# Performance work log

Measured on AMD Instinct MI355X. Metric: run time of the kernel, lower is better.

The kernel has to match this reference:

```python
import jax, jax.numpy as jnp
import numpy as np

# dims
D = 1024; H = 16; DH = D // H; FF = 4096; E = 4; K = 64; M = 256; B = 2; S = 1024
DEPTH = 1.0 + 12.0 / 24.0 * 0.5  # depth_factor for layer_idx=12, num_layers=24
SCALE = 1.0 / np.sqrt(DH)
GATE_DIM = 128


def _heads(t):
    # (B,S,D) -> (B,H,S,DH)
    return t.reshape(t.shape[0], t.shape[1], H, DH).transpose(0, 2, 1, 3)


def _merge(t):
    # (B,H,S,DH) -> (B,S,D)
    return t.transpose(0, 2, 1, 3).reshape(t.shape[0], t.shape[2], D)


def _ln(x, g, b):
    mu = x.mean(-1, keepdims=True)
    var = x.var(-1, keepdims=True)
    return (x - mu) / jnp.sqrt(var + 1e-5) * g + b


def _mha(x, wq, bq, wk, bk, wv, bv, wo, bo):
    q = _heads(x @ wq + bq); k = _heads(x @ wk + bk); v = _heads(x @ wv + bv)
    s = jnp.einsum('bhqd,bhkd->bhqk', q, k) * SCALE
    a = jax.nn.softmax(s, axis=-1)
    return _merge(jnp.einsum('bhqk,bhkd->bhqd', a, v)) @ wo + bo


def _sparse_mha(x, wq, bq, wk, bk, wv, bv, wo, bo):
    # DynamicSparseAttention: keep top-K scores per query, mask the rest
    q = _heads(x @ wq + bq); k = _heads(x @ wk + bk); v = _heads(x @ wv + bv)
    s = jnp.einsum('bhqd,bhkd->bhqk', q, k) * SCALE
    thr = jax.lax.top_k(s, K)[0][..., -1:]             # kth-largest per query
    s = jnp.where(s >= thr, s, -1e9)
    a = jax.nn.softmax(s, axis=-1)
    return _merge(jnp.einsum('bhqk,bhkd->bhqd', a, v)) @ wo + bo


def _performer(x, wq, bq, wk, bk, wv, bv, wo, bo, wf):
    # LearnedPerformerAttention: learned ReLU feature maps, linear attention
    q = _heads(x @ wq + bq); k = _heads(x @ wk + bk); v = _heads(x @ wv + bv)
    pq = jax.nn.relu(jnp.einsum('bhsd,dm->bhsm', q, wf))
    pk = jax.nn.relu(jnp.einsum('bhsd,dm->bhsm', k, wf))
    kv = jnp.einsum('bhsm,bhsd->bhmd', pk, v)          # (B,H,M,DH)
    z = pk.sum(axis=2)                                  # (B,H,M)
    num = jnp.einsum('bhsm,bhmd->bhsd', pq, kv)
    den = jnp.einsum('bhsm,bhm->bhs', pq, z) + 1e-6
    return _merge(num / den[..., None]) @ wo + bo


def setup_inputs() -> dict:
    key = jax.random.key(0)
    ks = iter(jax.random.split(key, 64))

    def w(shape):
        fan_in = shape[-2] if len(shape) > 1 else shape[-1]
        return (jax.random.normal(next(ks), shape, jnp.float32) / np.sqrt(fan_in))

    inp = {'x': jax.random.normal(next(ks), (B, S, D), jnp.float32)}
    # AdaptiveReasoningGate
    inp['arg_w1'] = w((D, GATE_DIM)); inp['arg_b1'] = jnp.zeros(GATE_DIM)
    inp['arg_w2'] = w((GATE_DIM, 2)); inp['arg_b2'] = jnp.zeros(2)
    # MoE attention: router + per-expert MHA
    inp['moe_wr'] = w((D, E)); inp['moe_br'] = jnp.zeros(E)
    for n in ('wq', 'wk', 'wv', 'wo'):
        inp['moe_' + n] = w((E, D, D))
        inp['moe_b' + n[1]] = jnp.zeros((E, D))
    # sparse attention
    for n in ('wq', 'wk', 'wv', 'wo'):
        inp['sp_' + n] = w((D, D)); inp['sp_b' + n[1]] = jnp.zeros(D)
    # performer attention
    for n in ('wq', 'wk', 'wv', 'wo'):
        inp['pf_' + n] = w((D, D)); inp['pf_b' + n[1]] = jnp.zeros(D)
    inp['pf_wf'] = w((DH, M))
    # TAA gate, attention combiner gate
    inp['taa_wg'] = w((D, 2)); inp['taa_bg'] = jnp.zeros(2)
    inp['ag_w'] = w((D, 2)); inp['ag_b'] = jnp.zeros(2)
    # FFN
    inp['ffn_w1'] = w((D, FF)); inp['ffn_b1'] = jnp.zeros(FF)
    inp['ffn_w2'] = w((FF, D)); inp['ffn_b2'] = jnp.zeros(D)
    # norms
    for i in (1, 2, 3):
        inp[f'n{i}_g'] = jnp.ones(D); inp[f'n{i}_b'] = jnp.zeros(D)
    return inp


def _forward(x, arg_w1, arg_b1, arg_w2, arg_b2,
             moe_wr, moe_br, moe_wq, moe_bq, moe_wk, moe_bk, moe_wv, moe_bv, moe_wo, moe_bo,
             sp_wq, sp_bq, sp_wk, sp_bk, sp_wv, sp_bv, sp_wo, sp_bo,
             pf_wq, pf_bq, pf_wk, pf_bk, pf_wv, pf_bv, pf_wo, pf_bo, pf_wf,
             taa_wg, taa_bg, ag_w, ag_b,
             ffn_w1, ffn_b1, ffn_w2, ffn_b2,
             n1_g, n1_b, n2_g, n2_b, n3_g, n3_b):
    avg = x.mean(axis=1)  # (B,D)
    # AdaptiveReasoningGate (attn_weight computed but unused in original forward)
    gw = jax.nn.sigmoid(jax.nn.gelu(avg @ arg_w1 + arg_b1) @ arg_w2 + arg_b2)
    ffn_weight = gw[:, 1][:, None, None]
    # MoE attention: token-level softmax routing over E expert MHAs
    ex_out = jax.vmap(
        lambda wq, bq, wk, bk, wv, bv, wo, bo: _mha(x, wq, bq, wk, bk, wv, bv, wo, bo)
    )(moe_wq, moe_bq, moe_wk, moe_bk, moe_wv, moe_bv, moe_wo, moe_bo)  # (E,B,S,D)
    gates = jax.nn.softmax(x @ moe_wr + moe_br, axis=-1)               # (B,S,E)
    moe_out = jnp.einsum('ebsd,bse->bsd', ex_out, gates)
    # Hybrid thought-aware attention (dropout = identity, eval mode)
    sp = _sparse_mha(x, sp_wq, sp_bq, sp_wk, sp_bk, sp_wv, sp_bv, sp_wo, sp_bo)
    pf = _performer(x, pf_wq, pf_bq, pf_wk, pf_bk, pf_wv, pf_bv, pf_wo, pf_bo, pf_wf)
    tg = jax.nn.softmax(avg @ taa_wg + taa_bg, axis=-1)
    taa_out = tg[:, 0][:, None, None] * sp + tg[:, 1][:, None, None] * pf
    # gated combine of MoE and TAA paths
    ag = jax.nn.softmax(avg @ ag_w + ag_b, axis=-1)
    attn_out = (ag[:, 0][:, None, None] * moe_out + ag[:, 1][:, None, None] * taa_out) * DEPTH
    x1 = _ln(x + attn_out, n1_g, n1_b)
    ffn_out = (jax.nn.gelu(x1 @ ffn_w1 + ffn_b1) @ ffn_w2 + ffn_b2) * ffn_weight * DEPTH
    x2 = _ln(x1 + ffn_out, n2_g, n2_b)
    return _ln(x2, n3_g, n3_b)


def reference(x, arg_w1, arg_b1, arg_w2, arg_b2,
              moe_wr, moe_br, moe_wq, moe_bq, moe_wk, moe_bk, moe_wv, moe_bv, moe_wo, moe_bo,
              sp_wq, sp_bq, sp_wk, sp_bk, sp_wv, sp_bv, sp_wo, sp_bo,
              pf_wq, pf_bq, pf_wk, pf_bk, pf_wv, pf_bv, pf_wo, pf_bo, pf_wf,
              taa_wg, taa_bg, ag_w, ag_b,
              ffn_w1, ffn_b1, ffn_w2, ffn_b2,
              n1_g, n1_b, n2_g, n2_b, n3_g, n3_b):
    return _forward(x, arg_w1, arg_b1, arg_w2, arg_b2,
                    moe_wr, moe_br, moe_wq, moe_bq, moe_wk, moe_bk, moe_wv, moe_bv, moe_wo, moe_bo,
                    sp_wq, sp_bq, sp_wk, sp_bk, sp_wv, sp_bv, sp_wo, sp_bo,
                    pf_wq, pf_bq, pf_wk, pf_bk, pf_wv, pf_bv, pf_wo, pf_bo, pf_wf,
                    taa_wg, taa_bg, ag_w, ag_b,
                    ffn_w1, ffn_b1, ffn_w2, ffn_b2,
                    n1_g, n1_b, n2_g, n2_b, n3_g, n3_b)
```

## Files before the change

### kernel.cpp

```cpp
#include <hip/hip_runtime.h>
#include <hip/hip_bf16.h>
#include <math.h>

#define Bq 2
#define Sq 1024
#define Dq 1024
#define Hq 16
#define DHq 64
#define FFq 4096
#define Eq 4
#define Kq 64
#define Mq 256
#define GATEq 128
#define BSq (Bq*Sq)
#define DEPTHF 1.25f
#define SCALEF 0.125f
#define DD (Dq*Dq)
#define PLANE ((size_t)BSq*Dq)

typedef __hip_bfloat16 bf16;
typedef __attribute__((ext_vector_type(8))) __bf16 bf16x8;
typedef __attribute__((ext_vector_type(4))) float f32x4;

__device__ __forceinline__ float toF(float v){ return v; }
__device__ __forceinline__ float toF(bf16 v){ return __bfloat162float(v); }
__device__ __forceinline__ void stF(float* p, size_t i, float v){ p[i] = v; }
__device__ __forceinline__ void stF(bf16* p, size_t i, float v){ p[i] = __float2bfloat16(v); }
__device__ __forceinline__ float gelu_f(float x){
  const float c = 0.7978845608028654f;
  return 0.5f*x*(1.0f + tanhf(c*(x + 0.044715f*x*x*x)));
}
__device__ __forceinline__ unsigned short bfb(float f){
  bf16 h = __float2bfloat16(f);
  return *(unsigned short*)&h;
}
__device__ __forceinline__ float thr_decode(unsigned c){
  unsigned ub = (c & 0x80000000u) ? (c & 0x7FFFFFFFu) : ~c;
  return __uint_as_float(ub);
}
__device__ __forceinline__ void async_lds16(const void* g, void* lds) {
  __builtin_amdgcn_global_load_lds(
      (const __attribute__((address_space(1))) void*)(unsigned long long)(uintptr_t)g,
      (__attribute__((address_space(3))) void*)(unsigned)(uintptr_t)lds, 16, 0, 0);
}

__global__ __launch_bounds__(256)
void detect_kernel(const unsigned* __restrict__ xw, int* __restrict__ flag)
{
  __shared__ int cnt;
  if (threadIdx.x == 0) cnt = 0;
  __syncthreads();
  int c = 0;
  for (int i = threadIdx.x; i < 4096; i += 256) {
    unsigned e = (xw[i] >> 7) & 0xFFu;
    c += (e >= 0x70u && e <= 0x8Fu) ? 1 : 0;
  }
#pragma unroll
  for (int o = 32; o >= 1; o >>= 1) c += __shfl_xor(c, o);
  if ((threadIdx.x & 63) == 0) atomicAdd(&cnt, c);
  __syncthreads();
  if (threadIdx.x == 0) *flag = (cnt > 2048) ? 1 : 0;
}

__global__ __launch_bounds__(256)
void conv_x_kernel(const int* __restrict__ flag, const void* __restrict__ x, bf16* __restrict__ xb)
{
  int f = *flag;
  int i0 = (blockIdx.x*256 + threadIdx.x)*4;
  if (i0 >= BSq*Dq) return;
  if (f) {
    const bf16* s = (const bf16*)x;
#pragma unroll
    for (int k=0;k<4;k++) xb[i0+k] = s[i0+k];
  } else {
    const float* s = (const float*)x;
#pragma unroll
    for (int k=0;k<4;k++) xb[i0+k] = __float2bfloat16(s[i0+k]);
  }
}

template<typename IT>
__device__ void packseg(bf16* dst, const IT* src, int len)
{
  for (int i = threadIdx.x; i < len; i += 256) dst[i] = __float2bfloat16(toF(src[i]));
}
__global__ __launch_bounds__(256)
void pack_bias_kernel(const int* __restrict__ flag, bf16* arena,
    const void* bq, const void* bk, const void* bv, const void* bo,
    const void* sq, const void* sk, const void* sv, const void* so,
    const void* pq, const void* pk, const void* pv, const void* po,
    const void* f1, const void* f2)
{
  int f = *flag;
  if (f) {
    packseg(arena+0,     (const bf16*)bq, 4096); packseg(arena+4096,  (const bf16*)bk, 4096);
    packseg(arena+8192,  (const bf16*)bv, 4096); packseg(arena+12288, (const bf16*)bo, 4096);
    packseg(arena+16384, (const bf16*)sq, 1024); packseg(arena+17408, (const bf16*)sk, 1024);
    packseg(arena+18432, (const bf16*)sv, 1024); packseg(arena+19456, (const bf16*)so, 1024);
    packseg(arena+20480, (const bf16*)pq, 1024); packseg(arena+21504, (const bf16*)pk, 1024);
    packseg(arena+22528, (const bf16*)pv, 1024); packseg(arena+23552, (const bf16*)po, 1024);
// ... 5 lines not shown
    packseg(arena+18432, (const float*)sv, 1024); packseg(arena+19456, (const float*)so, 1024);
    packseg(arena+20480, (const float*)pq, 1024); packseg(arena+21504, (const float*)pk, 1024);
    packseg(arena+22528, (const float*)pv, 1024); packseg(arena+23552, (const float*)po, 1024);
    packseg(arena+24576, (const float*)f1, 4096); packseg(arena+28672, (const float*)f2, 1024);
  }
}

template<typename IT>
__device__ void packwft_body(const IT* __restrict__ wf, bf16* __restrict__ wft)
{
  int i = blockIdx.x*256 + threadIdx.x;
  if (i >= DHq*Mq) return;
  int d = i >> 8, m = i & 255;
  wft[m*DHq + d] = __float2bfloat16(toF(wf[(size_t)d*Mq + m]));
}
__global__ __launch_bounds__(256)
void pack_wft_kernel(const int* __restrict__ flag, const void* wf, bf16* wft)
{
  if (*flag) packwft_body<bf16>((const bf16*)wf, wft);
  else       packwft_body<float>((const float*)wf, wft);
}

template<typename WT>
__device__ void gemm_core(bf16* As, unsigned* Bs,
    const bf16* __restrict__ A, int lda, const WT* __restrict__ W,
    const bf16* __restrict__ barena, int biasOff,
    const float* __restrict__ rowscale, bf16* __restrict__ C,
    float* __restrict__ Cf, int N, int K, int act)
{
  int tid = threadIdx.x;
  int lane = tid & 63, wave = tid >> 6;
  int wr = wave >> 1, wc = wave & 1;
  int bm = blockIdx.x * 128, bn = blockIdx.y * 128;

  int arow1 = wave*16 + (lane>>2);
  int akey = (arow1 >> 1) & 3;
  int acol = ((lane & 3) ^ akey) * 8;
  const bf16* aP1 = A + (size_t)(bm + arow1)*lda + acol;
  const bf16* aP2 = A + (size_t)(bm + arow1 + 64)*lda + acol;

  int kp = tid >> 4, nb8 = (tid & 15)*8;
  const WT* wP = W + (size_t)(2*kp)*N + bn + nb8;

  f32x4 acc[4][4];
#pragma unroll
  for (int i=0;i<4;i++)
#pragma unroll
    for (int j=0;j<4;j++) acc[i][j] = (f32x4){0.f,0.f,0.f,0.f};

  int m = lane & 15, q = lane >> 4;
  int akey2 = (m >> 1) & 3;
  int aq = (q ^ akey2) * 8;

  const int T = K >> 5;
  uint4 rwa, rwb, rwc, rwd;

// ... 76 lines not shown
#pragma unroll
  for (int i=0;i<4;i++) {
    int row0 = bm + wr*64 + i*16 + q*4;
#pragma unroll
    for (int j=0;j<4;j++) {
      int col = bn + wc*64 + j*16 + m;
      float bvv = barena ? toF(barena[biasOff + col]) : 0.f;
#pragma unroll
      for (int r=0;r<4;r++) {
        size_t idx = (size_t)(row0 + r)*N + col;
        if (Cf) {
          Cf[idx] = acc[i][j][r];
        } else {
          float v = acc[i][j][r] + bvv;
          if (act) v = gelu_f(v);
          if (rowscale) v *= rowscale[row0 + r];
          C[idx] = __float2bfloat16(v);
        }
      }
    }
  }
}

__global__ __launch_bounds__(256, 3)
void gemm6_k(const int* __restrict__ flag, const bf16* Abase, long az,
    const void* w0, const void* w1, const void* w2,
    const void* w3, const void* w4, const void* w5,
    long e0, long e1, long e2, long e3, long e4, long e5,
    int b0, int b1, int b2, int b3, int b4, int b5,
    const float* r0, const float* r1, const float* r2,
    const float* r3, const float* r4, const float* r5,
    bf16* c0, bf16* c1, bf16* c2, bf16* c3, bf16* c4, bf16* c5,
    const bf16* barena, int N, int K)
{
  __shared__ bf16 As[2*4096];
  __shared__ unsigned Bs[2*2112];
  int z = blockIdx.z;
  const void* Wp = (z==0)?w0:(z==1)?w1:(z==2)?w2:(z==3)?w3:(z==4)?w4:w5;
  long eo        = (z==0)?e0:(z==1)?e1:(z==2)?e2:(z==3)?e3:(z==4)?e4:e5;
  int bo         = (z==0)?b0:(z==1)?b1:(z==2)?b2:(z==3)?b3:(z==4)?b4:b5;
  const float* rs= (z==0)?r0:(z==1)?r1:(z==2)?r2:(z==3)?r3:(z==4)?r4:r5;
  bf16* C        = (z==0)?c0:(z==1)?c1:(z==2)?c2:(z==3)?c3:(z==4)?c4:c5;
  const bf16* A  = Abase + (size_t)z*az;
  if (*flag) gemm_core<bf16>(As, Bs, A, K, (const bf16*)Wp + eo, barena, bo, rs, C, nullptr, N, K, 0);
  else       gemm_core<float>(As, Bs, A, K, (const float*)Wp + eo, barena, bo, rs, C, nullptr, N, K, 0);
}

__global__ __launch_bounds__(256, 3)
void gemm1_k(const int* __restrict__ flag, const bf16* A, int lda, const void* W,
             const bf16* barena, int biasOff, const float* rowscale,
             bf16* C, float* Cf, long cfz, int N, int K, int act, int kz)
{
  __shared__ bf16 As[2*4096];
  __shared__ unsigned Bs[2*2112];
  int z = blockIdx.z;
  const bf16* Az = A + (size_t)z*kz;
  long wo = (size_t)z*kz*N;
  float* Cfz = Cf ? (Cf + (size_t)z*cfz) : nullptr;
  if (*flag) gemm_core<bf16>(As, Bs, Az, lda, (const bf16*)W + wo, barena, biasOff, rowscale, C, Cfz, N, K, act);
  else       gemm_core<float>(As, Bs, Az, lda, (const float*)W + wo, barena, biasOff, rowscale, C, Cfz, N, K, act);
}

__global__ __launch_bounds__(256)
void combine_ffn2(const float* __restrict__ pf, const bf16* __restrict__ barena,
                  const float* __restrict__ rs, bf16* __restrict__ out)
{
  int i0 = (blockIdx.x*256 + threadIdx.x)*4;
  float4 s0 = *(const float4*)(pf + i0);
  float4 s1 = *(const float4*)(pf + PLANE + i0);
  float4 s2 = *(const float4*)(pf + 2*PLANE + i0);
  float4 s3 = *(const float4*)(pf + 3*PLANE + i0);
  int row = i0 >> 10, col = i0 & 1023;
  float r = rs[row];
  out[i0+0] = __float2bfloat16((s0.x+s1.x+s2.x+s3.x + toF(barena[28672+col+0])) * r);
  out[i0+1] = __float2bfloat16((s0.y+s1.y+s2.y+s3.y + toF(barena[28672+col+1])) * r);
  out[i0+2] = __float2bfloat16((s0.z+s1.z+s2.z+s3.z + toF(barena[28672+col+2])) * r);
  out[i0+3] = __float2bfloat16((s0.w+s1.w+s2.w+s3.w + toF(barena[28672+col+3])) * r);
}

__global__ __launch_bounds__(256)
void vtrans_kernel(const bf16* __restrict__ Vb, long vz, bf16* __restrict__ Vtb, long vtz)
{
  __shared__ bf16 t[64][72];
  const bf16* V = Vb + (size_t)blockIdx.z*vz;
  bf16* Vt = Vtb + (size_t)blockIdx.z*vtz;
  int bh = blockIdx.x;
  int sc_ = blockIdx.y;
  int b = bh >> 4, h = bh & 15;
  int tid = threadIdx.x;
  {
    int s = tid >> 2, dd = (tid & 3) * 16;
    const bf16* src = &V[((size_t)b*Sq + sc_*64 + s)*Dq + h*64 + dd];
    uint4 a0 = *(const uint4*)src;
    uint4 a1 = *(const uint4*)(src + 8);
    *(uint4*)&t[s][dd]     = a0;
    *(uint4*)&t[s][dd + 8] = a1;
  }
  __syncthreads();
  {
    int d = tid >> 2, sp = (tid & 3) * 16;
// ... 118 lines not shown
  lrun += __shfl_xor(lrun, 32);
#pragma unroll
  for (int dt=0;dt<4;dt++)
    *(float4*)&ocs[wave][m][dt*16 + q*4] = (float4){oc[dt][0], oc[dt][1], oc[dt][2], oc[dt][3]};
  if (q == 0) { mls[wave][0][m] = mrun; mls[wave][1][m] = lrun; }
  __syncthreads();

  int mm = tid >> 4, d0 = (tid & 15) * 4;
  float m0 = mls[0][0][mm], m1 = mls[1][0][mm], m2 = mls[2][0][mm], m3 = mls[3][0][mm];
  float M = fmaxf(fmaxf(m0, m1), fmaxf(m2, m3));
  float a0 = __expf(m0 - M), a1 = __expf(m1 - M), a2 = __expf(m2 - M), a3 = __expf(m3 - M);
  float l = mls[0][1][mm]*a0 + mls[1][1][mm]*a1 + mls[2][1][mm]*a2 + mls[3][1][mm]*a3;
  l = fmaxf(l, 1e-30f);
  float inv = 1.0f / l;
  float4 o0 = *(const float4*)&ocs[0][mm][d0];
  float4 o1 = *(const float4*)&ocs[1][mm][d0];
  float4 o2 = *(const float4*)&ocs[2][mm][d0];
  float4 o3 = *(const float4*)&ocs[3][mm][d0];
  float r0 = (o0.x*a0 + o1.x*a1 + o2.x*a2 + o3.x*a3) * inv;
  float r1 = (o0.y*a0 + o1.y*a1 + o2.y*a2 + o3.y*a3) * inv;
  float r2 = (o0.z*a0 + o1.z*a1 + o2.z*a2 + o3.z*a3) * inv;
  float r3 = (o0.w*a0 + o1.w*a1 + o2.w*a2 + o3.w*a3) * inv;
  bf16* op = O + base + (size_t)(q0 + mm)*Dq + d0;
  unsigned w0 = (unsigned)bfb(r0) | ((unsigned)bfb(r1) << 16);
  unsigned w1 = (unsigned)bfb(r2) | ((unsigned)bfb(r3) << 16);
  *(uint2*)op = make_uint2(w0, w1);
}

template<int SPARSE>
__global__ __launch_bounds__(256, 4)
void attn_kernel(const bf16* __restrict__ Q, const bf16* __restrict__ K,
                 const bf16* __restrict__ Vt, bf16* __restrict__ O)
{
  const int PAST = 1032;
  __shared__ bf16 pa[16*PAST];
  __shared__ float partA[64], partB[64];
  __shared__ int cntb[2][64];

  int p_ = blockIdx.x;
  int g_ = (p_ & 7)*4 + ((p_ >> 3) & 3);
  int rb = p_ >> 5;
  int h  = g_ & 15;
  int b  = g_ >> 4;
  int tid = threadIdx.x, lane = tid & 63, wave = tid >> 6;
  int m = lane & 15, q = lane >> 4;
  size_t base = ((size_t)b*Sq)*Dq + (size_t)h*DHq;
  int q0 = rb*16;

  const bf16* qrow = &Q[base + (size_t)(q0+m)*Dq + q*8];
  bf16x8 aq0 = *(const bf16x8*)qrow;
  bf16x8 aq1 = *(const bf16x8*)(qrow + 32);

  f32x4 cc[16];
#pragma unroll
  for (int t = 0; t < 16; t++) {
    int j0 = wave*256 + t*16;
    const bf16* kp = &K[base + (size_t)(j0+m)*Dq + q*8];
    bf16x8 b0 = *(const bf16x8*)kp;
    bf16x8 b1 = *(const bf16x8*)(kp + 32);
    f32x4 c = {0.f,0.f,0.f,0.f};
    c = __builtin_amdgcn_mfma_f32_16x16x32_bf16(aq0, b0, c, 0, 0, 0);
    c = __builtin_amdgcn_mfma_f32_16x16x32_bf16(aq1, b1, c, 0, 0, 0);
#pragma unroll
    for (int r=0;r<4;r++) c[r] *= SCALEF;
    cc[t] = c;
  }

  unsigned lo[4] = {0u,0u,0u,0u};
  if (SPARSE) {
    int cnt_cur[4] = {Sq, Sq, Sq, Sq};
    for (int bit = 31; bit >= 0; bit--) {
      int par = bit & 1;
      unsigned cand[4];
      float candf[4];
      int c4[4] = {0,0,0,0};
#pragma unroll
      for (int r=0;r<4;r++) {
        cand[r] = lo[r] | (1u << bit);
        candf[r] = thr_decode(cand[r]);
      }
#pragma unroll
      for (int t=0;t<16;t++)
#pragma unroll
        for (int r=0;r<4;r++) c4[r] += (cc[t][r] >= candf[r]) ? 1 : 0;
#pragma unroll
      for (int o=1;o<16;o<<=1)
#pragma unroll
        for (int r=0;r<4;r++) c4[r] += __shfl_xor(c4[r], o);
      if (m == 0) {
#pragma unroll
        for (int r=0;r<4;r++) cntb[par][wave*16 + q*4 + r] = c4[r];
      }
      __syncthreads();
      int done = 1;
#pragma unroll
      for (int r=0;r<4;r++) {
        int row = q*4 + r;
        int tot = cntb[par][row] + cntb[par][16+row] + cntb[par][32+row] + cntb[par][48+row];
        if (tot >= Kq) { lo[r] = cand[r]; cnt_cur[r] = tot; }
        done &= (cnt_cur[r] == Kq) ? 1 : 0;
      }
      done &= __shfl_xor(done, 16);
      done &= __shfl_xor(done, 32);
      if (done) break;
    }
  }

  float mrow[4];
#pragma unroll
  for (int r=0;r<4;r++) {
    float v = -1e30f;
#pragma unroll
    for (int t=0;t<16;t++) v = fmaxf(v, cc[t][r]);
#pragma unroll
    for (int o=1;o<16;o<<=1) v = fmaxf(v, __shfl_xor(v, o));
    mrow[r] = v;
  }
  if (m == 0) {
#pragma unroll
    for (int r=0;r<4;r++) partA[wave*16 + q*4 + r] = mrow[r];
  }
  __syncthreads();
// ... 207 lines not shown

  const bf16* kvp = kvb + (size_t)bh*(DHq*Mq);
  f32x4 oc[4];
#pragma unroll
  for (int dt=0;dt<4;dt++) oc[dt] = (f32x4){0.f,0.f,0.f,0.f};
#pragma unroll
  for (int ks=0; ks<8; ks++) {
    bf16x8 ap = *(const bf16x8*)&pa2[(wave*16 + ml)*PQST + ks*32 + q*8];
#pragma unroll
    for (int dt=0;dt<4;dt++) {
      bf16x8 bk = *(const bf16x8*)&kvp[(size_t)(dt*16 + ml)*Mq + ks*32 + q*8];
      oc[dt] = __builtin_amdgcn_mfma_f32_16x16x32_bf16(ap, bk, oc[dt], 0, 0, 0);
    }
  }
#pragma unroll
  for (int dt=0;dt<4;dt++)
#pragma unroll
    for (int r=0;r<4;r++)
      O[base + (size_t)(s0 + wave*16 + q*4 + r)*Dq + dt*16 + ml] =
          __float2bfloat16(oc[dt][r] / den[r]);
}

template<typename IT>
__device__ void ln_body(float* buf, float* red, const IT* __restrict__ xb,
                        const void* Ap, const void* Bp,
                        const IT* __restrict__ g, const IT* __restrict__ be,
                        void* out, int mode)
{
  int row = blockIdx.x;
  int tid = threadIdx.x;
  size_t off = (size_t)row*Dq;
  for (int dd = tid; dd < Dq; dd += 256) {
    float v;
    if (mode == 0)      v = toF(xb[off+dd]) + toF(((const bf16*)Ap)[off+dd]);
    else if (mode == 1) v = toF(((const bf16*)Ap)[off+dd]) + toF(((const bf16*)Bp)[off+dd]);
    else if (mode == 3) {
      const bf16* P = (const bf16*)Ap;
      v = toF(xb[off+dd]);
#pragma unroll
      for (int p=0;p<6;p++) v += toF(P[(size_t)p*PLANE + off + dd]);
    }
    else                v = toF(((const bf16*)Ap)[off+dd]);
    buf[dd] = v;
  }
  __syncthreads();
  float s = 0.f, q = 0.f;
  for (int dd = tid; dd < Dq; dd += 256) { float v = buf[dd]; s += v; q += v*v; }
#pragma unroll
  for (int o=32;o>=1;o>>=1) { s += __shfl_xor(s,o); q += __shfl_xor(q,o); }
  int w = tid >> 6;
  if ((tid & 63) == 0) { red[w] = s; red[4+w] = q; }
  __syncthreads();
  if (tid == 0) {
    float S1 = red[0]+red[1]+red[2]+red[3];
    float Q1 = red[4]+red[5]+red[6]+red[7];
    float mu = S1 / (float)Dq;
    float var = Q1 / (float)Dq - mu*mu;
    red[8] = mu; red[9] = rsqrtf(fmaxf(var, 0.f) + 1e-5f);
  }
  __syncthreads();
  float mu = red[8], inv = red[9];
  for (int dd = tid; dd < Dq; dd += 256) {
    float v = (buf[dd]-mu)*inv*toF(g[dd]) + toF(be[dd]);
    if (mode == 2) stF((IT*)out, off+dd, v);
    else           stF((bf16*)out, off+dd, v);
  }
}

__global__ __launch_bounds__(256)
void ln_kernel(const int* __restrict__ flag, const void* xb, const void* A, const void* Bv,
               const void* g, const void* be, void* out, int mode)
{
  __shared__ float buf[Dq];
  __shared__ float red[10];
  if (*flag) ln_body<bf16>(buf, red, (const bf16*)xb, A, Bv, (const bf16*)g, (const bf16*)be, out, mode);
  else       ln_body<float>(buf, red, (const float*)xb, A, Bv, (const float*)g, (const float*)be, out, mode);
}

__global__ __launch_bounds__(256)
void avg2_kernel(const int* __restrict__ flag, const void* __restrict__ x, float* __restrict__ avgsum)
{
  int b  = blockIdx.x >> 4;
  int sc = blockIdx.x & 15;
  int t = threadIdx.x;
  int c0 = t*4;
  float a0=0.f,a1=0.f,a2=0.f,a3=0.f;
  if (*flag) {
    const unsigned* X = (const unsigned*)x;
    for (int s = sc*64; s < sc*64+64; s++) {
      size_t bi = (((size_t)(b*Sq + s))*Dq + c0) >> 1;
      unsigned u0 = X[bi], u1 = X[bi+1];
      a0 += __uint_as_float(u0 << 16);
      a1 += __uint_as_float(u0 & 0xFFFF0000u);
      a2 += __uint_as_float(u1 << 16);
      a3 += __uint_as_float(u1 & 0xFFFF0000u);
    }
  } else {
    const float* X = (const float*)x;
    for (int s = sc*64; s < sc*64+64; s++) {
// ... 83 lines not shown
    float ag0 = f0*inv, ag1 = f1*inv;
    cmb0[b] = ag0*DEPTHF;
    sh[2+b] = tg0*ag1*DEPTHF;
    sh[4+b] = tg1*ag1*DEPTHF;
    sh[6+b] = sh[b]*DEPTHF;
  }
  __syncthreads();
  for (int i = tid; i < BSq; i += 256) {
    int b = i >> 10;
    rs_tg0[i] = sh[2+b]; rs_tg1[i] = sh[4+b]; rs_ffn[i] = sh[6+b];
  }
}
__global__ __launch_bounds__(256)
void gate_fin_kernel(const int* __restrict__ flag, const float* g1b, const float* lgb,
    const void* w2, const void* b2, float* cmb0,
    float* rs_tg0, float* rs_tg1, float* rs_ffn)
{
  __shared__ float sh[8];
  if (*flag) gfin_body<bf16>(sh, g1b, lgb, (const bf16*)w2, (const bf16*)b2, cmb0, rs_tg0, rs_tg1, rs_ffn);
  else       gfin_body<float>(sh, g1b, lgb, (const float*)w2, (const float*)b2, cmb0, rs_tg0, rs_tg1, rs_ffn);
}

template<typename IT>
__device__ void router_body(const IT* __restrict__ x, const IT* __restrict__ wr,
                            const IT* __restrict__ br, const float* __restrict__ cmb0,
                            float* __restrict__ gates_t)
{
  int row = blockIdx.x;
  int tid = threadIdx.x;
  size_t off = (size_t)row*Dq;
  float a0=0,a1=0,a2=0,a3=0;
  for (int dd = tid; dd < Dq; dd += 64) {
    float xv = toF(x[off+dd]);
    a0 += xv*toF(wr[dd*Eq+0]);
    a1 += xv*toF(wr[dd*Eq+1]);
    a2 += xv*toF(wr[dd*Eq+2]);
    a3 += xv*toF(wr[dd*Eq+3]);
  }
#pragma unroll
  for (int o=32;o>=1;o>>=1) {
    a0 += __shfl_xor(a0,o); a1 += __shfl_xor(a1,o);
    a2 += __shfl_xor(a2,o); a3 += __shfl_xor(a3,o);
  }
  if (tid == 0) {
    a0 += toF(br[0]); a1 += toF(br[1]); a2 += toF(br[2]); a3 += toF(br[3]);
    float m = fmaxf(fmaxf(a0,a1),fmaxf(a2,a3));
    float e0=__expf(a0-m), e1=__expf(a1-m), e2=__expf(a2-m), e3=__expf(a3-m);
    float inv = 1.f/(e0+e1+e2+e3);
    float sc = cmb0[row >> 10];
    gates_t[0*BSq+row]=e0*inv*sc; gates_t[1*BSq+row]=e1*inv*sc;
    gates_t[2*BSq+row]=e2*inv*sc; gates_t[3*BSq+row]=e3*inv*sc;
  }
}
__global__ __launch_bounds__(64)
void router_kernel(const int* __restrict__ flag, const void* x, const void* wr,
                   const void* br, const float* cmb0, float* gates_t)
{
  if (*flag) router_body<bf16>((const bf16*)x, (const bf16*)wr, (const bf16*)br, cmb0, gates_t);
  else       router_body<float>((const float*)x, (const float*)wr, (const float*)br, cmb0, gates_t);
}

extern "C" void kernel_launch(void* const* d_in, const int* in_sizes, int n_in,
                              void* d_out, int out_size, void* d_ws, size_t ws_size,
                              hipStream_t stream) {
  const void* x      = d_in[0];
  const void* arg_w1 = d_in[1];  const void* arg_b1 = d_in[2];
  const void* arg_w2 = d_in[3];  const void* arg_b2 = d_in[4];
  const void* moe_wr = d_in[5];  const void* moe_br = d_in[6];
  const void* moe_wq = d_in[7];  const void* moe_bq = d_in[8];
  const void* moe_wk = d_in[9];  const void* moe_bk = d_in[10];
  const void* moe_wv = d_in[11]; const void* moe_bv = d_in[12];
  const void* moe_wo = d_in[13]; const void* moe_bo = d_in[14];
  const void* sp_wq  = d_in[15]; const void* sp_bq  = d_in[16];
  const void* sp_wk  = d_in[17]; const void* sp_bk  = d_in[18];
  const void* sp_wv  = d_in[19]; const void* sp_bv  = d_in[20];
  const void* sp_wo  = d_in[21]; const void* sp_bo  = d_in[22];
  const void* pf_wq  = d_in[23]; const void* pf_bq  = d_in[24];
  const void* pf_wk  = d_in[25]; const void* pf_bk  = d_in[26];
  const void* pf_wv  = d_in[27]; const void* pf_bv  = d_in[28];
  const void* pf_wo  = d_in[29]; const void* pf_bo  = d_in[30];
  const void* pf_wf  = d_in[31];
  const void* taa_wg = d_in[32]; const void* taa_bg = d_in[33];
  const void* ag_w   = d_in[34]; const void* ag_b   = d_in[35];
  const void* ffn_w1 = d_in[36]; const void* ffn_b1 = d_in[37];
  const void* ffn_w2 = d_in[38]; const void* ffn_b2 = d_in[39];
  const void* n1_g   = d_in[40]; const void* n1_b   = d_in[41];
  const void* n2_g   = d_in[42]; const void* n2_b   = d_in[43];
  const void* n3_g   = d_in[44]; const void* n3_b   = d_in[45];

  char* w = (char*)d_ws;
  const size_t MB = 1024*1024;
  bf16* xb  = (bf16*)w;
  bf16* Qp  = (bf16*)(w + 4*MB);
  bf16* KV  = (bf16*)(w + 28*MB);
  bf16* Vt  = (bf16*)(w + 44*MB);
  bf16* Pp  = (bf16*)(w + 28*MB);
  bf16* x1    = (bf16*)(w + 4*MB);
  bf16* ffn_h = (bf16*)(w + 8*MB);
  float* partF= (float*)(w + 24*MB);
  bf16* tmpb  = (bf16*)w;
  bf16* x2    = (bf16*)w;
  char* book = w + 56*MB;
  float* rs_tg0 = (float*)book;
  float* rs_tg1 = rs_tg0 + BSq;
  float* rs_ffn = rs_tg1 + BSq;
  float* cmb0   = rs_ffn + BSq;
  float* avgp   = cmb0 + 16;
  float* gates_t= avgp + Bq*Dq;
  float* zb     = gates_t + Eq*BSq;
  float* g1b    = zb + Bq*Hq*Mq;
  float* lgb    = g1b + 256;
  int*   dflag  = (int*)(lgb + 8);
  bf16*  barena = (bf16*)(dflag + 16);
  bf16*  wft    = barena + 29696;
  bf16*  kvb    = (bf16*)(w + 57*MB);

  detect_kernel<<<1, 256, 0, stream>>>((const unsigned*)x, dflag);
  hipMemsetAsync(avgp, 0, (size_t)(Bq*Dq)*sizeof(float), stream);
  conv_x_kernel<<<BSq*Dq/1024, 256, 0, stream>>>(dflag, x, xb);
  pack_bias_kernel<<<1, 256, 0, stream>>>(dflag, barena,
      moe_bq, moe_bk, moe_bv, moe_bo, sp_bq, sp_bk, sp_bv, sp_bo,
      pf_bq, pf_bk, pf_bv, pf_bo, ffn_b1, ffn_b2);
  pack_wft_kernel<<<64, 256, 0, stream>>>(dflag, pf_wf, wft);
  avg2_kernel<<<Bq*16, 256, 0, stream>>>(dflag, x, avgp);
  gate_dots_kernel<<<66, 256, 0, stream>>>(dflag, avgp, arg_w1, arg_b1,
      taa_wg, taa_bg, ag_w, ag_b, g1b, lgb);
  gate_fin_kernel<<<1, 256, 0, stream>>>(dflag, g1b, lgb, arg_w2, arg_b2,
      cmb0, rs_tg0, rs_tg1, rs_ffn);
  router_kernel<<<BSq, 64, 0, stream>>>(dflag, x, moe_wr, moe_br, cmb0, gates_t);

  dim3 g6(16, 8, 6);
  dim3 gVT(Bq*Hq, Sq/64, 2);
  int nAttnBlk = Bq*Hq*(Sq/16);
  int nFlashBlk = Bq*Hq*(Sq/16);

  for (int p = 0; p < 2; p++) {
    int e0 = 2*p, e1 = 2*p + 1;
    gemm6_k<<<g6, 256, 0, stream>>>(dflag, xb, 0L,
        moe_wq, moe_wk, moe_wv, moe_wq, moe_wk, moe_wv,
        (long)e0*DD, (long)e0*DD, (long)e0*DD, (long)e1*DD, (long)e1*DD, (long)e1*DD,
        e0*1024, e0*1024+4096, e0*1024+8192, e1*1024, e1*1024+4096, e1*1024+8192,
        nullptr, nullptr, nullptr, nullptr, nullptr, nullptr,
        Qp + (size_t)e0*PLANE, KV, KV + PLANE,
        Qp + (size_t)e1*PLANE, KV + 2*PLANE, KV + 3*PLANE,
        barena, Dq, Dq);
    vtrans_kernel<<<gVT, 256, 0, stream>>>(KV + PLANE, (long)(2*PLANE), Vt, (long)PLANE);
    flash_attn_kernel<<<nFlashBlk, 256, 0, stream>>>(Qp + (size_t)e0*PLANE, KV, Vt, Qp + (size_t)e0*PLANE);
    flash_attn_kernel<<<nFlashBlk, 256, 0, stream>>>(Qp + (size_t)e1*PLANE, KV + 2*PLANE, Vt + PLANE, Qp + (size_t)e1*PLANE);
  }

  gemm6_k<<<g6, 256, 0, stream>>>(dflag, xb, 0L,
      sp_wq, sp_wk, sp_wv, pf_wq, pf_wk, pf_wv,
      0L, 0L, 0L, 0L, 0L, 0L,
      16384, 17408, 18432, 20480, 21504, 22528,
      nullptr, nullptr, nullptr, nullptr, nullptr, nullptr,
      Qp + 4*PLANE, KV, KV + PLANE,
      Qp + 5*PLANE, KV + 2*PLANE, KV + 3*PLANE,
      barena, Dq, Dq);
  vtrans_kernel<<<gVT, 256, 0, stream>>>(KV + PLANE, (long)(2*PLANE), Vt, (long)PLANE);
  attn_kernel<1><<<nAttnBlk, 256, 0, stream>>>(Qp + 4*PLANE, KV, Vt, Qp + 4*PLANE);
  {
    dim3 gKV1(Bq*Hq, 8);
    perf_kv_mfma<<<gKV1, 256, 0, stream>>>(KV + 2*PLANE, Vt + PLANE, wft, kvb, zb);
  }
  perf_out_mfma<<<Bq*Hq*16, 256, 0, stream>>>(Qp + 5*PLANE, wft, kvb, zb, Qp + 5*PLANE);

  gemm6_k<<<g6, 256, 0, stream>>>(dflag, Qp, (long)PLANE,
      moe_wo, moe_wo, moe_wo, moe_wo, sp_wo, pf_wo,
      0L, (long)DD, (long)2*DD, (long)3*DD, 0L, 0L,
      12288, 13312, 14336, 15360, 19456, 23552,
      gates_t, gates_t + BSq, gates_t + 2*BSq, gates_t + 3*BSq, rs_tg0, rs_tg1,
      Pp, Pp + PLANE, Pp + 2*PLANE, Pp + 3*PLANE, Pp + 4*PLANE, Pp + 5*PLANE,
      barena, Dq, Dq);

  ln_kernel<<<BSq, 256, 0, stream>>>(dflag, x, Pp, nullptr, n1_g, n1_b, x1, 3);

  gemm1_k<<<dim3(16, 32, 1), 256, 0, stream>>>(dflag, x1, Dq, ffn_w1,
      barena, 24576, nullptr, ffn_h, nullptr, 0L, FFq, Dq, 1, 0);
  gemm1_k<<<dim3(16, 8, 4), 256, 0, stream>>>(dflag, ffn_h, FFq, ffn_w2,
      nullptr, 0, nullptr, nullptr, partF, (long)PLANE, Dq, 1024, 0, 1024);
  combine_ffn2<<<BSq*Dq/1024, 256, 0, stream>>>(partF, barena, rs_ffn, tmpb);

  ln_kernel<<<BSq, 256, 0, stream>>>(dflag, nullptr, x1, tmpb, n2_g, n2_b, x2, 1);
  ln_kernel<<<BSq, 256, 0, stream>>>(dflag, nullptr, x2, nullptr, n3_g, n3_b, d_out, 2);
}
```

Baseline: 1.092 ms.

## Fuse FFN tail layernorms, swizzle GEMM tiles across XCDs, radix-4 top-k search

Several independent changes land together. The FFN2 partial-sum combine and the two final layernorms merge into one kernel, which removes intermediate bf16 round trips and two launches. GEMM blocks are remapped so each XCD works on contiguous panels for better L2 reuse. The sparse attention threshold search now tests two bits per pass with three candidates, halving the sync rounds. LN1, the router and the x conversion are also vectorized with 4-wide loads and stores. Dropping the bf16 intermediate between FFN add and LN2 slightly changes numerics.

```diff
diff --git a/kernel.cpp b/kernel.cpp
--- a/kernel.cpp
+++ b/kernel.cpp
@@ -24,8 +24,6 @@
 
 __device__ __forceinline__ float toF(float v){ return v; }
 __device__ __forceinline__ float toF(bf16 v){ return __bfloat162float(v); }
-__device__ __forceinline__ void stF(float* p, size_t i, float v){ p[i] = v; }
-__device__ __forceinline__ void stF(bf16* p, size_t i, float v){ p[i] = __float2bfloat16(v); }
 __device__ __forceinline__ float gelu_f(float x){
   const float c = 0.7978845608028654f;
   return 0.5f*x*(1.0f + tanhf(c*(x + 0.044715f*x*x*x)));
@@ -33,6 +31,25 @@
 __device__ __forceinline__ unsigned short bfb(float f){
   bf16 h = __float2bfloat16(f);
   return *(unsigned short*)&h;
+}
+__device__ __forceinline__ uint2 pack4bf(float a, float b, float c, float d){
+  return make_uint2((unsigned)bfb(a) | ((unsigned)bfb(b) << 16),
+                    (unsigned)bfb(c) | ((unsigned)bfb(d) << 16));
+}
+template<typename IT>
+__device__ __forceinline__ void ld4(const IT* p, float* o){
+  if constexpr (sizeof(IT)==4){
+    float4 v = *(const float4*)p; o[0]=v.x; o[1]=v.y; o[2]=v.z; o[3]=v.w;
+  } else {
+    uint2 u = *(const uint2*)p;
+    o[0]=__uint_as_float(u.x<<16); o[1]=__uint_as_float(u.x&0xFFFF0000u);
+    o[2]=__uint_as_float(u.y<<16); o[3]=__uint_as_float(u.y&0xFFFF0000u);
+  }
+}
+template<typename IT>
+__device__ __forceinline__ void st4(IT* p, const float* v){
+  if constexpr (sizeof(IT)==4){ *(float4*)p = (float4){v[0],v[1],v[2],v[3]}; }
+  else { *(uint2*)p = pack4bf(v[0],v[1],v[2],v[3]); }
 }
 __device__ __forceinline__ float thr_decode(unsigned c){
   unsigned ub = (c & 0x80000000u) ? (c & 0x7FFFFFFFu) : ~c;
@@ -65,17 +82,13 @@
 __global__ __launch_bounds__(256)
 void conv_x_kernel(const int* __restrict__ flag, const void* __restrict__ x, bf16* __restrict__ xb)
 {
-  int f = *flag;
   int i0 = (blockIdx.x*256 + threadIdx.x)*4;
   if (i0 >= BSq*Dq) return;
-  if (f) {
-    const bf16* s = (const bf16*)x;
-#pragma unroll
-    for (int k=0;k<4;k++) xb[i0+k] = s[i0+k];
+  if (*flag) {
+    *(uint2*)(xb + i0) = *(const uint2*)((const bf16*)x + i0);
   } else {
-    const float* s = (const float*)x;
-#pragma unroll
-    for (int k=0;k<4;k++) xb[i0+k] = __float2bfloat16(s[i0+k]);
+    float4 v = *(const float4*)((const float*)x + i0);
+    *(uint2*)(xb + i0) = pack4bf(v.x, v.y, v.z, v.w);
   }
 }
 
@@ -127,7 +140,7 @@
 }
 
 template<typename WT>
-__device__ void gemm_core(bf16* As, unsigned* Bs,
+__device__ void gemm_core(bf16* As, unsigned* Bs, int bm, int bn,
     const bf16* __restrict__ A, int lda, const WT* __restrict__ W,
     const bf16* __restrict__ barena, int biasOff,
     const float* __restrict__ rowscale, bf16* __restrict__ C,
@@ -136,7 +149,6 @@
   int tid = threadIdx.x;
   int lane = tid & 63, wave = tid >> 6;
   int wr = wave >> 1, wc = wave & 1;
-  int bm = blockIdx.x * 128, bn = blockIdx.y * 128;
 
   int arow1 = wave*16 + (lane>>2);
   int akey = (arow1 >> 1) & 3;
@@ -259,6 +271,19 @@
   }
 }
 
+__device__ __forceinline__ void xcd_swizzle(int& xt, int& y, int& z)
+{
+  int nx = gridDim.x, ny = gridDim.y, nz = gridDim.z;
+  int lin = blockIdx.x + nx*(blockIdx.y + ny*blockIdx.z);
+  int ppx = (ny*nz) >> 3;
+  int xcd = lin & 7, sdx = lin >> 3;
+  int pp = sdx / nx;
+  xt = sdx - pp*nx;
+  int panel = xcd*ppx + pp;
+  y = panel % ny;
+  z = panel / ny;
+}
+
 __global__ __launch_bounds__(256, 3)
 void gemm6_k(const int* __restrict__ flag, const bf16* Abase, long az,
     const void* w0, const void* w1, const void* w2,
@@ -272,15 +297,16 @@
 {
   __shared__ bf16 As[2*4096];
   __shared__ unsigned Bs[2*2112];
-  int z = blockIdx.z;
+  int xt, y, z;
+  xcd_swizzle(xt, y, z);
   const void* Wp = (z==0)?w0:(z==1)?w1:(z==2)?w2:(z==3)?w3:(z==4)?w4:w5;
   long eo        = (z==0)?e0:(z==1)?e1:(z==2)?e2:(z==3)?e3:(z==4)?e4:e5;
   int bo         = (z==0)?b0:(z==1)?b1:(z==2)?b2:(z==3)?b3:(z==4)?b4:b5;
   const float* rs= (z==0)?r0:(z==1)?r1:(z==2)?r2:(z==3)?r3:(z==4)?r4:r5;
   bf16* C        = (z==0)?c0:(z==1)?c1:(z==2)?c2:(z==3)?c3:(z==4)?c4:c5;
   const bf16* A  = Abase + (size_t)z*az;
-  if (*flag) gemm_core<bf16>(As, Bs, A, K, (const bf16*)Wp + eo, barena, bo, rs, C, nullptr, N, K, 0);
-  else       gemm_core<float>(As, Bs, A, K, (const float*)Wp + eo, barena, bo, rs, C, nullptr, N, K, 0);
+  if (*flag) gemm_core<bf16>(As, Bs, xt*128, y*128, A, K, (const bf16*)Wp + eo, barena, bo, rs, C, nullptr, N, K, 0);
+  else       gemm_core<float>(As, Bs, xt*128, y*128, A, K, (const float*)Wp + eo, barena, bo, rs, C, nullptr, N, K, 0);
 }
 
 __global__ __launch_bounds__(256, 3)
@@ -290,29 +316,13 @@
 {
   __shared__ bf16 As[2*4096];
   __shared__ unsigned Bs[2*2112];
-  int z = blockIdx.z;
+  int xt, y, z;
+  xcd_swizzle(xt, y, z);
   const bf16* Az = A + (size_t)z*kz;
   long wo = (size_t)z*kz*N;
   float* Cfz = Cf ? (Cf + (size_t)z*cfz) : nullptr;
-  if (*flag) gemm_core<bf16>(As, Bs, Az, lda, (const bf16*)W + wo, barena, biasOff, rowscale, C, Cfz, N, K, act);
-  else       gemm_core<float>(As, Bs, Az, lda, (const float*)W + wo, barena, biasOff, rowscale, C, Cfz, N, K, act);
-}
-
-__global__ __launch_bounds__(256)
-void combine_ffn2(const float* __restrict__ pf, const bf16* __restrict__ barena,
-                  const float* __restrict__ rs, bf16* __restrict__ out)
-{
-  int i0 = (blockIdx.x*256 + threadIdx.x)*4;
-  float4 s0 = *(const float4*)(pf + i0);
-  float4 s1 = *(const float4*)(pf + PLANE + i0);
-  float4 s2 = *(const float4*)(pf + 2*PLANE + i0);
-  float4 s3 = *(const float4*)(pf + 3*PLANE + i0);
-  int row = i0 >> 10, col = i0 & 1023;
-  float r = rs[row];
-  out[i0+0] = __float2bfloat16((s0.x+s1.x+s2.x+s3.x + toF(barena[28672+col+0])) * r);
-  out[i0+1] = __float2bfloat16((s0.y+s1.y+s2.y+s3.y + toF(barena[28672+col+1])) * r);
-  out[i0+2] = __float2bfloat16((s0.z+s1.z+s2.z+s3.z + toF(barena[28672+col+2])) * r);
-  out[i0+3] = __float2bfloat16((s0.w+s1.w+s2.w+s3.w + toF(barena[28672+col+3])) * r);
+  if (*flag) gemm_core<bf16>(As, Bs, xt*128, y*128, Az, lda, (const bf16*)W + wo, barena, biasOff, rowscale, C, Cfz, N, K, act);
+  else       gemm_core<float>(As, Bs, xt*128, y*128, Az, lda, (const float*)W + wo, barena, biasOff, rowscale, C, Cfz, N, K, act);
 }
 
 __global__ __launch_bounds__(256)
@@ -477,9 +487,7 @@
   float r2 = (o0.z*a0 + o1.z*a1 + o2.z*a2 + o3.z*a3) * inv;
   float r3 = (o0.w*a0 + o1.w*a1 + o2.w*a2 + o3.w*a3) * inv;
   bf16* op = O + base + (size_t)(q0 + mm)*Dq + d0;
-  unsigned w0 = (unsigned)bfb(r0) | ((unsigned)bfb(r1) << 16);
-  unsigned w1 = (unsigned)bfb(r2) | ((unsigned)bfb(r3) << 16);
-  *(uint2*)op = make_uint2(w0, w1);
+  *(uint2*)op = pack4bf(r0, r1, r2, r3);
 }
 
 template<int SPARSE>
@@ -490,7 +498,7 @@
   const int PAST = 1032;
   __shared__ bf16 pa[16*PAST];
   __shared__ float partA[64], partB[64];
-  __shared__ int cntb[2][64];
+  __shared__ int cntb[2][192];
 
   int p_ = blockIdx.x;
   int g_ = (p_ & 7)*4 + ((p_ >> 3) & 3);
@@ -524,35 +532,50 @@
   unsigned lo[4] = {0u,0u,0u,0u};
   if (SPARSE) {
     int cnt_cur[4] = {Sq, Sq, Sq, Sq};
-    for (int bit = 31; bit >= 0; bit--) {
-      int par = bit & 1;
-      unsigned cand[4];
-      float candf[4];
-      int c4[4] = {0,0,0,0};
+    for (int bit = 30; bit >= 0; bit -= 2) {
+      int par = (bit >> 1) & 1;
+      float cf[4][3];
+      unsigned cd[4][3];
+      int cnt[4][3];
 #pragma unroll
       for (int r=0;r<4;r++) {
-        cand[r] = lo[r] | (1u << bit);
-        candf[r] = thr_decode(cand[r]);
+        cd[r][0] = lo[r] | (3u << bit);
+        cd[r][1] = lo[r] | (2u << bit);
+        cd[r][2] = lo[r] | (1u << bit);
+#pragma unroll
+        for (int c=0;c<3;c++) { cf[r][c] = thr_decode(cd[r][c]); cnt[r][c] = 0; }
       }
 #pragma unroll
       for (int t=0;t<16;t++)
 #pragma unroll
-        for (int r=0;r<4;r++) c4[r] += (cc[t][r] >= candf[r]) ? 1 : 0;
+        for (int r=0;r<4;r++) {
+          float v = cc[t][r];
+#pragma unroll
+          for (int c=0;c<3;c++) cnt[r][c] += (v >= cf[r][c]) ? 1 : 0;
+        }
 #pragma unroll
       for (int o=1;o<16;o<<=1)
 #pragma unroll
-        for (int r=0;r<4;r++) c4[r] += __shfl_xor(c4[r], o);
+        for (int r=0;r<4;r++)
+#pragma unroll
+          for (int c=0;c<3;c++) cnt[r][c] += __shfl_xor(cnt[r][c], o);
       if (m == 0) {
 #pragma unroll
-        for (int r=0;r<4;r++) cntb[par][wave*16 + q*4 + r] = c4[r];
+        for (int r=0;r<4;r++)
+#pragma unroll
+          for (int c=0;c<3;c++) cntb[par][c*64 + wave*16 + q*4 + r] = cnt[r][c];
       }
       __syncthreads();
       int done = 1;
 #pragma unroll
       for (int r=0;r<4;r++) {
         int row = q*4 + r;
-        int tot = cntb[par][row] + cntb[par][16+row] + cntb[par][32+row] + cntb[par][48+row];
-        if (tot >= Kq) { lo[r] = cand[r]; cnt_cur[r] = tot; }
+        int n3 = cntb[par][row] + cntb[par][16+row] + cntb[par][32+row] + cntb[par][48+row];
+        int n2 = cntb[par][64+row] + cntb[par][80+row] + cntb[par][96+row] + cntb[par][112+row];
+        int n1 = cntb[par][128+row] + cntb[par][144+row] + cntb[par][160+row] + cntb[par][176+row];
+        if      (n3 >= Kq) { lo[r] = cd[r][0]; cnt_cur[r] = n3; }
+        else if (n2 >= Kq) { lo[r] = cd[r][1]; cnt_cur[r] = n2; }
+        else if (n1 >= Kq) { lo[r] = cd[r][2]; cnt_cur[r] = n1; }
         done &= (cnt_cur[r] == Kq) ? 1 : 0;
       }
       done &= __shfl_xor(done, 16);
@@ -806,36 +829,29 @@
 }
 
 template<typename IT>
-__device__ void ln_body(float* buf, float* red, const IT* __restrict__ xb,
-                        const void* Ap, const void* Bp,
-                        const IT* __restrict__ g, const IT* __restrict__ be,
-                        void* out, int mode)
-{
-  int row = blockIdx.x;
-  int tid = threadIdx.x;
-  size_t off = (size_t)row*Dq;
-  for (int dd = tid; dd < Dq; dd += 256) {
-    float v;
-    if (mode == 0)      v = toF(xb[off+dd]) + toF(((const bf16*)Ap)[off+dd]);
-    else if (mode == 1) v = toF(((const bf16*)Ap)[off+dd]) + toF(((const bf16*)Bp)[off+dd]);
-    else if (mode == 3) {
-      const bf16* P = (const bf16*)Ap;
-      v = toF(xb[off+dd]);
-#pragma unroll
-      for (int p=0;p<6;p++) v += toF(P[(size_t)p*PLANE + off + dd]);
-    }
-    else                v = toF(((const bf16*)Ap)[off+dd]);
-    buf[dd] = v;
-  }
-  __syncthreads();
-  float s = 0.f, q = 0.f;
-  for (int dd = tid; dd < Dq; dd += 256) { float v = buf[dd]; s += v; q += v*v; }
-#pragma unroll
-  for (int o=32;o>=1;o>>=1) { s += __shfl_xor(s,o); q += __shfl_xor(q,o); }
-  int w = tid >> 6;
-  if ((tid & 63) == 0) { red[w] = s; red[4+w] = q; }
-  __syncthreads();
-  if (tid == 0) {
+__device__ void ln1_body(float* red, const IT* __restrict__ xsrc, const bf16* __restrict__ Pp,
+                         const IT* __restrict__ g, const IT* __restrict__ be, bf16* __restrict__ out)
+{
+  int row = blockIdx.x, t = threadIdx.x;
+  int c0 = t*4;
+  size_t off = (size_t)row*Dq + c0;
+  float v[4];
+  ld4(xsrc + off, v);
+#pragma unroll
+  for (int p=0;p<6;p++) {
+    float pv[4];
+    ld4(Pp + (size_t)p*PLANE + off, pv);
+#pragma unroll
+    for (int j=0;j<4;j++) v[j] += pv[j];
+  }
+  float s = v[0]+v[1]+v[2]+v[3];
+  float qq = v[0]*v[0]+v[1]*v[1]+v[2]*v[2]+v[3]*v[3];
+#pragma unroll
+  for (int o=32;o>=1;o>>=1) { s += __shfl_xor(s,o); qq += __shfl_xor(qq,o); }
+  int w = t >> 6;
+  if ((t & 63) == 0) { red[w] = s; red[4+w] = qq; }
+  __syncthreads();
+  if (t == 0) {
     float S1 = red[0]+red[1]+red[2]+red[3];
     float Q1 = red[4]+red[5]+red[6]+red[7];
     float mu = S1 / (float)Dq;
@@ -844,21 +860,97 @@
   }
   __syncthreads();
   float mu = red[8], inv = red[9];
-  for (int dd = tid; dd < Dq; dd += 256) {
-    float v = (buf[dd]-mu)*inv*toF(g[dd]) + toF(be[dd]);
-    if (mode == 2) stF((IT*)out, off+dd, v);
-    else           stF((bf16*)out, off+dd, v);
-  }
-}
-
-__global__ __launch_bounds__(256)
-void ln_kernel(const int* __restrict__ flag, const void* xb, const void* A, const void* Bv,
-               const void* g, const void* be, void* out, int mode)
-{
-  __shared__ float buf[Dq];
+  float gv[4], bv[4];
+  ld4(g + c0, gv); ld4(be + c0, bv);
+  float o_[4];
+#pragma unroll
+  for (int j=0;j<4;j++) o_[j] = (v[j]-mu)*inv*gv[j] + bv[j];
+  *(uint2*)(out + off) = pack4bf(o_[0], o_[1], o_[2], o_[3]);
+}
+__global__ __launch_bounds__(256)
+void ln1_kernel(const int* __restrict__ flag, const void* xsrc, const bf16* Pp,
+                const void* g, const void* be, bf16* out)
+{
   __shared__ float red[10];
-  if (*flag) ln_body<bf16>(buf, red, (const bf16*)xb, A, Bv, (const bf16*)g, (const bf16*)be, out, mode);
-  else       ln_body<float>(buf, red, (const float*)xb, A, Bv, (const float*)g, (const float*)be, out, mode);
+  if (*flag) ln1_body<bf16>(red, (const bf16*)xsrc, Pp, (const bf16*)g, (const bf16*)be, out);
+  else       ln1_body<float>(red, (const float*)xsrc, Pp, (const float*)g, (const float*)be, out);
+}
+
+template<typename IT>
+__device__ void ffntail_body(float* red, const float* __restrict__ pf,
+    const bf16* __restrict__ barena, const float* __restrict__ rs,
+    const bf16* __restrict__ x1,
+    const IT* __restrict__ g2, const IT* __restrict__ b2,
+    const IT* __restrict__ g3, const IT* __restrict__ b3, IT* __restrict__ out)
+{
+  int row = blockIdx.x, t = threadIdx.x;
+  int c0 = t*4;
+  size_t off = (size_t)row*Dq + c0;
+  float4 s0 = *(const float4*)(pf + off);
+  float4 s1 = *(const float4*)(pf + PLANE + off);
+  float4 s2 = *(const float4*)(pf + 2*PLANE + off);
+  float4 s3 = *(const float4*)(pf + 3*PLANE + off);
+  float bb[4]; ld4(barena + 28672 + c0, bb);
+  float xv[4]; ld4(x1 + off, xv);
+  float r = rs[row];
+  float v[4];
+  v[0] = xv[0] + (s0.x+s1.x+s2.x+s3.x + bb[0])*r;
+  v[1] = xv[1] + (s0.y+s1.y+s2.y+s3.y + bb[1])*r;
+  v[2] = xv[2] + (s0.z+s1.z+s2.z+s3.z + bb[2])*r;
+  v[3] = xv[3] + (s0.w+s1.w+s2.w+s3.w + bb[3])*r;
+  float s = v[0]+v[1]+v[2]+v[3];
+  float qq = v[0]*v[0]+v[1]*v[1]+v[2]*v[2]+v[3]*v[3];
+#pragma unroll
+  for (int o=32;o>=1;o>>=1) { s += __shfl_xor(s,o); qq += __shfl_xor(qq,o); }
+  int w = t >> 6;
+  if ((t & 63) == 0) { red[w] = s; red[4+w] = qq; }
+  __syncthreads();
+  if (t == 0) {
+    float S1 = red[0]+red[1]+red[2]+red[3];
+    float Q1 = red[4]+red[5]+red[6]+red[7];
+    float mu = S1 / (float)Dq;
+    float var = Q1 / (float)Dq - mu*mu;
+    red[8] = mu; red[9] = rsqrtf(fmaxf(var, 0.f) + 1e-5f);
+  }
+  __syncthreads();
+  float mu = red[8], inv = red[9];
+  float g2v[4], b2v[4];
+  ld4(g2 + c0, g2v); ld4(b2 + c0, b2v);
+  float y[4];
+#pragma unroll
+  for (int j=0;j<4;j++) y[j] = (v[j]-mu)*inv*g2v[j] + b2v[j];
+  float s2_ = y[0]+y[1]+y[2]+y[3];
+  float q2_ = y[0]*y[0]+y[1]*y[1]+y[2]*y[2]+y[3]*y[3];
+#pragma unroll
+  for (int o=32;o>=1;o>>=1) { s2_ += __shfl_xor(s2_,o); q2_ += __shfl_xor(q2_,o); }
+  if ((t & 63) == 0) { red[10+w] = s2_; red[14+w] = q2_; }
+  __syncthreads();
+  if (t == 0) {
+    float S1 = red[10]+red[11]+red[12]+red[13];
+    float Q1 = red[14]+red[15]+red[16]+red[17];
+    float mu2 = S1 / (float)Dq;
+    float var2 = Q1 / (float)Dq - mu2*mu2;
+    red[18] = mu2; red[19] = rsqrtf(fmaxf(var2, 0.f) + 1e-5f);
+  }
+  __syncthreads();
+  float mu2 = red[18], inv2 = red[19];
+  float g3v[4], b3v[4];
+  ld4(g3 + c0, g3v); ld4(b3 + c0, b3v);
+  float o_[4];
+#pragma unroll
+  for (int j=0;j<4;j++) o_[j] = (y[j]-mu2)*inv2*g3v[j] + b3v[j];
+  st4(out + off, o_);
+}
+__global__ __launch_bounds__(256)
+void ffn_tail_kernel(const int* __restrict__ flag, const float* pf, const bf16* barena,
+    const float* rs, const bf16* x1, const void* g2, const void* b2,
+    const void* g3, const void* b3, void* out)
+{
+  __shared__ float red[20];
+  if (*flag) ffntail_body<bf16>(red, pf, barena, rs, x1, (const bf16*)g2, (const bf16*)b2,
+                                (const bf16*)g3, (const bf16*)b3, (bf16*)out);
+  else       ffntail_body<float>(red, pf, barena, rs, x1, (const float*)g2, (const float*)b2,
+                                 (const float*)g3, (const float*)b3, (float*)out);
 }
 
 __global__ __launch_bounds__(256)
@@ -988,27 +1080,59 @@
 }
 
 template<typename IT>
-__device__ void router_body(const IT* __restrict__ x, const IT* __restrict__ wr,
-                            const IT* __restrict__ br, const float* __restrict__ cmb0,
-                            float* __restrict__ gates_t)
-{
-  int row = blockIdx.x;
-  int tid = threadIdx.x;
-  size_t off = (size_t)row*Dq;
-  float a0=0,a1=0,a2=0,a3=0;
-  for (int dd = tid; dd < Dq; dd += 64) {
-    float xv = toF(x[off+dd]);
-    a0 += xv*toF(wr[dd*Eq+0]);
-    a1 += xv*toF(wr[dd*Eq+1]);
-    a2 += xv*toF(wr[dd*Eq+2]);
-    a3 += xv*toF(wr[dd*Eq+3]);
+__device__ void router2_body(const IT* __restrict__ x, const IT* __restrict__ wr,
+                             const IT* __restrict__ br, const float* __restrict__ cmb0,
+                             float* __restrict__ gates_t)
+{
+  int tid = threadIdx.x, lane = tid & 63, wave = tid >> 6;
+  int row = blockIdx.x*4 + wave;
+  float a0=0.f,a1=0.f,a2=0.f,a3=0.f;
+  if constexpr (sizeof(IT)==4) {
+    const float* xf = (const float*)x + (size_t)row*Dq;
+    const float* wf = (const float*)wr;
+#pragma unroll
+    for (int rr=0; rr<4; rr++) {
+      int dd0 = rr*256 + lane*4;
+      float4 xv = *(const float4*)&xf[dd0];
+      float xa[4] = {xv.x, xv.y, xv.z, xv.w};
+#pragma unroll
+      for (int j=0;j<4;j++) {
+        float4 wv = *(const float4*)&wf[(size_t)(dd0+j)*4];
+        a0 += xa[j]*wv.x; a1 += xa[j]*wv.y; a2 += xa[j]*wv.z; a3 += xa[j]*wv.w;
+      }
+    }
+  } else {
+    const unsigned* xu = (const unsigned*)((const bf16*)x + (size_t)row*Dq);
+    const unsigned* wu = (const unsigned*)wr;
+#pragma unroll
+    for (int rr=0; rr<2; rr++) {
+      int dd0 = rr*512 + lane*8;
+      uint4 xv = *(const uint4*)&xu[dd0>>1];
+      unsigned xw[4] = {xv.x, xv.y, xv.z, xv.w};
+#pragma unroll
+      for (int p=0;p<4;p++) {
+        float x0 = __uint_as_float(xw[p] << 16);
+        float x1v = __uint_as_float(xw[p] & 0xFFFF0000u);
+        int dd = dd0 + p*2;
+        uint2 w0 = *(const uint2*)&wu[(size_t)dd*2];
+        uint2 w1 = *(const uint2*)&wu[(size_t)(dd+1)*2];
+        a0 += x0*__uint_as_float(w0.x<<16);
+        a1 += x0*__uint_as_float(w0.x&0xFFFF0000u);
+        a2 += x0*__uint_as_float(w0.y<<16);
+        a3 += x0*__uint_as_float(w0.y&0xFFFF0000u);
+        a0 += x1v*__uint_as_float(w1.x<<16);
+        a1 += x1v*__uint_as_float(w1.x&0xFFFF0000u);
+        a2 += x1v*__uint_as_float(w1.y<<16);
+        a3 += x1v*__uint_as_float(w1.y&0xFFFF0000u);
+      }
+    }
   }
 #pragma unroll
   for (int o=32;o>=1;o>>=1) {
     a0 += __shfl_xor(a0,o); a1 += __shfl_xor(a1,o);
     a2 += __shfl_xor(a2,o); a3 += __shfl_xor(a3,o);
   }
-  if (tid == 0) {
+  if (lane == 0) {
     a0 += toF(br[0]); a1 += toF(br[1]); a2 += toF(br[2]); a3 += toF(br[3]);
     float m = fmaxf(fmaxf(a0,a1),fmaxf(a2,a3));
     float e0=__expf(a0-m), e1=__expf(a1-m), e2=__expf(a2-m), e3=__expf(a3-m);
@@ -1018,12 +1142,12 @@
     gates_t[2*BSq+row]=e2*inv*sc; gates_t[3*BSq+row]=e3*inv*sc;
   }
 }
-__global__ __launch_bounds__(64)
-void router_kernel(const int* __restrict__ flag, const void* x, const void* wr,
-                   const void* br, const float* cmb0, float* gates_t)
-{
-  if (*flag) router_body<bf16>((const bf16*)x, (const bf16*)wr, (const bf16*)br, cmb0, gates_t);
-  else       router_body<float>((const float*)x, (const float*)wr, (const float*)br, cmb0, gates_t);
+__global__ __launch_bounds__(256)
+void router2_kernel(const int* __restrict__ flag, const void* x, const void* wr,
+                    const void* br, const float* cmb0, float* gates_t)
+{
+  if (*flag) router2_body<bf16>((const bf16*)x, (const bf16*)wr, (const bf16*)br, cmb0, gates_t);
+  else       router2_body<float>((const float*)x, (const float*)wr, (const float*)br, cmb0, gates_t);
 }
 
 extern "C" void kernel_launch(void* const* d_in, const int* in_sizes, int n_in,
@@ -1064,8 +1188,6 @@
   bf16* x1    = (bf16*)(w + 4*MB);
   bf16* ffn_h = (bf16*)(w + 8*MB);
   float* partF= (float*)(w + 24*MB);
-  bf16* tmpb  = (bf16*)w;
-  bf16* x2    = (bf16*)w;
   char* book = w + 56*MB;
   float* rs_tg0 = (float*)book;
   float* rs_tg1 = rs_tg0 + BSq;
@@ -1093,7 +1215,7 @@
       taa_wg, taa_bg, ag_w, ag_b, g1b, lgb);
   gate_fin_kernel<<<1, 256, 0, stream>>>(dflag, g1b, lgb, arg_w2, arg_b2,
       cmb0, rs_tg0, rs_tg1, rs_ffn);
-  router_kernel<<<BSq, 64, 0, stream>>>(dflag, x, moe_wr, moe_br, cmb0, gates_t);
+  router2_kernel<<<BSq/4, 256, 0, stream>>>(dflag, x, moe_wr, moe_br, cmb0, gates_t);
 
   dim3 g6(16, 8, 6);
   dim3 gVT(Bq*Hq, Sq/64, 2);
@@ -1139,14 +1261,13 @@
       Pp, Pp + PLANE, Pp + 2*PLANE, Pp + 3*PLANE, Pp + 4*PLANE, Pp + 5*PLANE,
       barena, Dq, Dq);
 
-  ln_kernel<<<BSq, 256, 0, stream>>>(dflag, x, Pp, nullptr, n1_g, n1_b, x1, 3);
+  ln1_kernel<<<BSq, 256, 0, stream>>>(dflag, x, Pp, n1_g, n1_b, x1);
 
   gemm1_k<<<dim3(16, 32, 1), 256, 0, stream>>>(dflag, x1, Dq, ffn_w1,
       barena, 24576, nullptr, ffn_h, nullptr, 0L, FFq, Dq, 1, 0);
   gemm1_k<<<dim3(16, 8, 4), 256, 0, stream>>>(dflag, ffn_h, FFq, ffn_w2,
       nullptr, 0, nullptr, nullptr, partF, (long)PLANE, Dq, 1024, 0, 1024);
-  combine_ffn2<<<BSq*Dq/1024, 256, 0, stream>>>(partF, barena, rs_ffn, tmpb);
-
-  ln_kernel<<<BSq, 256, 0, stream>>>(dflag, nullptr, x1, tmpb, n2_g, n2_b, x2, 1);
-  ln_kernel<<<BSq, 256, 0, stream>>>(dflag, nullptr, x2, nullptr, n3_g, n3_b, d_out, 2);
-}
+
+  ffn_tail_kernel<<<BSq, 256, 0, stream>>>(dflag, partF, barena, rs_ffn, x1,
+      n2_g, n2_b, n3_g, n3_b, d_out);
+}
```

Measured after the change: 1.116 ms. 2.2% more time.
